# Performance work log

Hardware: AMD Instinct MI355X
Metric: run time of the kernel (lower is better)

The kernel has to match this reference:

```python
import jax, jax.numpy as jnp
import numpy as np

B, N, F_IN = 4, 2048, 256
K, D = 4, 64
NEG_SLOPE = 0.2


def setup_inputs() -> dict:
    key = jax.random.key(0)
    k1, k2, k3, k4, k5 = jax.random.split(key, 5)
    x = jax.random.normal(k1, (B, N, F_IN), dtype=jnp.float32)
    adj = jax.random.randint(k2, (B, N, N), 0, 2, dtype=jnp.int32)
    # xavier_uniform-style params
    def xavier(k, shape):
        fan_in, fan_out = shape[-2], shape[-1]
        lim = np.sqrt(6.0 / (fan_in + fan_out))
        return jax.random.uniform(k, shape, jnp.float32, -lim, lim)
    W = xavier(k3, (K, F_IN, D))
    a_src = xavier(k4, (K, D, 1))
    a_dst = xavier(k5, (K, D, 1))
    return {"x": x, "adj": adj, "W": W, "a_src": a_src, "a_dst": a_dst}


def reference(x, adj, W, a_src, a_dst):
    # Wh: (B, K, N, D)
    Wh = jnp.einsum('bnf,kfd->bknd', x, W)
    e_src = jnp.einsum('bknd,kdo->bkno', Wh, a_src)  # (B,K,N,1)
    e_dst = jnp.einsum('bknd,kdo->bkno', Wh, a_dst)  # (B,K,N,1)
    e = e_src + jnp.swapaxes(e_dst, -2, -1)          # (B,K,N,N)
    e = jnp.where(e > 0, e, NEG_SLOPE * e)           # LeakyReLU(0.2)
    # adjacency mask with forced self-loops (adj + I > 0)
    eye = jnp.eye(e.shape[-1], dtype=bool)
    mask = (adj[:, None, :, :] > 0) | eye            # (B,1|K,N,N)
    e = jnp.where(mask, e, -jnp.inf)
    # numerically-stable softmax matching F_module_softmax
    x_max = jnp.max(e, axis=-1, keepdims=True)
    x_max = jnp.where(jnp.isinf(x_max), 0.0, x_max)
    exp_e = jnp.exp(e - x_max)
    exp_e = jnp.where(jnp.isinf(e), 0.0, exp_e)
    alpha = exp_e / (jnp.sum(exp_e, axis=-1, keepdims=True) + 1e-10)
    # dropout is identity in eval mode
    out = jnp.matmul(alpha, Wh)                      # (B,K,N,D)
    # concat heads: (B,N,K*D)
    Bn, Kn, Nn, Dn = out.shape
    return jnp.transpose(out, (0, 2, 1, 3)).reshape(Bn, Nn, Kn * Dn)
```

## Files before the change

### kernel.cpp

```cpp
#include <hip/hip_runtime.h>

#define NB 4
#define NN 2048
#define NF 256
#define NK 4
#define ND 64
#define NEG 0.2f
#define LOG2E 1.4426950408889634f

typedef _Float16 f16;
typedef _Float16 f16x2 __attribute__((ext_vector_type(2)));
typedef _Float16 f16x4 __attribute__((ext_vector_type(4)));
typedef _Float16 f16x8 __attribute__((ext_vector_type(8)));
typedef float f32x4 __attribute__((ext_vector_type(4)));
typedef float f32x16 __attribute__((ext_vector_type(16)));
typedef unsigned int u32;
typedef unsigned short u16;

__global__ __launch_bounds__(256) void k01(
    const float* __restrict__ x,
    const int*   __restrict__ adj,
    const float* __restrict__ Wm,
    const float* __restrict__ a_src,
    const float* __restrict__ a_dst,
    unsigned int* __restrict__ abit,
    f16* __restrict__ wht,
    float* __restrict__ sbuf,
    f16* __restrict__ ebuf,
    f16* __restrict__ fbuf)
{
    __shared__ f16 wt[64 * 256];

    const int bx  = blockIdx.x;
    const int tid = threadIdx.x;

    if (bx >= 256) {
        const int row = (bx - 256) * 4 + (tid >> 6);
        const int l   = tid & 63;
        const int i   = row & (NN - 1);
        const int* __restrict__ ar = adj + (size_t)row * NN;

        int v[32];
#pragma unroll
        for (int c = 0; c < 32; ++c) v[c] = ar[c * 64 + l];

        unsigned int kx = 0, ky = 0;
#pragma unroll
        for (int c = 0; c < 32; ++c) {
            unsigned long long m = __ballot(v[c] > 0);
            if (l == c) { kx = (unsigned int)m; ky = (unsigned int)(m >> 32); }
        }
        if (l == (i >> 6)) {
            unsigned int sb = 1u << (i & 31);
            if (((i >> 5) & 1) == 0) kx |= sb; else ky |= sb;
        }
        if (l < 32) {
            uint2 kk; kk.x = kx; kk.y = ky;
            *(uint2*)&abit[(size_t)row * 64 + l * 2] = kk;
        }
        return;
    }

    const int gx  = bx & 15;
    const int k   = (bx >> 4) & 3;
    const int b   = bx >> 6;
    const int wv  = tid >> 6;
    const int l   = tid & 63;
    const int q   = l >> 4;
    const int r16 = l & 15;

    for (int fc = 0; fc < 64; ++fc) {
        int f = fc * 4 + wv;
        int d = l;
        wt[d * 256 + (f ^ ((d & 7) << 3))] = (f16)Wm[(k * NF + f) * ND + d];
    }
    __syncthreads();

    const int ncol0 = gx * 128 + wv * 32;
    f32x4 acc[2][4];
#pragma unroll
    for (int nt = 0; nt < 2; ++nt)
#pragma unroll
        for (int dt = 0; dt < 4; ++dt)
            acc[nt][dt] = (f32x4){0.f, 0.f, 0.f, 0.f};

    for (int fs = 0; fs < 16; ++fs) {
        const int f0 = fs * 16 + q * 4;
        f16x4 af[4];
#pragma unroll
        for (int dt = 0; dt < 4; ++dt) {
            int d = dt * 16 + r16;
            af[dt] = *(const f16x4*)&wt[d * 256 + (f0 ^ ((d & 7) << 3))];
        }
#pragma unroll
        for (int nt = 0; nt < 2; ++nt) {
            int n = ncol0 + nt * 16 + r16;
            float4 xv = *(const float4*)&x[((size_t)(b * NN + n)) * NF + f0];
            f16x4 bf = {(f16)xv.x, (f16)xv.y, (f16)xv.z, (f16)xv.w};
#pragma unroll
            for (int dt = 0; dt < 4; ++dt)
                acc[nt][dt] = __builtin_amdgcn_mfma_f32_16x16x16f16(
                    af[dt], bf, acc[nt][dt], 0, 0, 0);
        }
    }

    float asv[4][4], adv[4][4];
#pragma unroll
    for (int dt = 0; dt < 4; ++dt)
#pragma unroll
        for (int rr = 0; rr < 4; ++rr) {
            int d = dt * 16 + q * 4 + rr;
            asv[dt][rr] = a_src[k * ND + d];
            adv[dt][rr] = a_dst[k * ND + d];
        }

    const size_t obase = (size_t)(b * NK + k) * 131072;

#pragma unroll
    for (int nt = 0; nt < 2; ++nt) {
        int n  = ncol0 + nt * 16 + r16;
        const size_t sb_ = obase + (size_t)(n >> 3) * 512 + (n & 7);
        float sp = 0.f, tp = 0.f;
#pragma unroll
        for (int dt = 0; dt < 4; ++dt)
#pragma unroll
            for (int rr = 0; rr < 4; ++rr) {
                float v = acc[nt][dt][rr];
                int d = dt * 16 + q * 4 + rr;
                wht[sb_ + d * 8] = (f16)v;
                sp += v * asv[dt][rr];
                tp += v * adv[dt][rr];
            }
        sp += __shfl_xor(sp, 16);
        sp += __shfl_xor(sp, 32);
        tp += __shfl_xor(tp, 16);
        tp += __shfl_xor(tp, 32);
        if (q == 0) {
            int idx = (b * NK + k) * NN + n;
            sbuf[idx] = sp;
            ebuf[idx] = (f16)__builtin_exp2f(tp * LOG2E);
            fbuf[idx] = (f16)__builtin_exp2f(0.2f * LOG2E * tp);
        }
    }
}

__global__ __launch_bounds__(512, 4) void k2_attn(
    const unsigned int* __restrict__ abit,
    const f16* __restrict__ wht,
    const float* __restrict__ sbuf,
    const f16* __restrict__ ebuf,
    const f16* __restrict__ fbuf,
    float* __restrict__ out)
{
    const int bid = blockIdx.x;
    const int bkv = (bid & 7) | (((bid >> 3) & 1) << 3);
    const int rg  = bid >> 4;
    const int b   = bkv >> 2, k = bkv & 3;
    const int i0  = rg * 64;
    const int tid = threadIdx.x;
    const int w   = tid >> 6;
    const int c   = w >> 1;
    const int rw  = w & 1;
    const int l   = tid & 63;
    const int r32 = l & 31;
    const int hi  = l >> 5;
    const int iglob = i0 + rw * 32 + r32;

    __shared__ __attribute__((aligned(16))) char pool[74752];
    u16* el = (u16*)(pool + 65536);
    u16* fl = (u16*)(pool + 69632);

    const unsigned int* __restrict__ abrow =
        abit + (size_t)(b * NN + iglob) * 64 + c * 16;
    uint2 abx[8];
#pragma unroll
    for (int it = 0; it < 8; ++it) abx[it] = *(const uint2*)(abrow + it * 2);

    {
        const u16* eb = (const u16*)(ebuf + bkv * NN);
        const u16* fb = (const u16*)(fbuf + bkv * NN);
        *(ushort4*)&el[tid * 4] = *(const ushort4*)&eb[tid * 4];
        *(ushort4*)&fl[tid * 4] = *(const ushort4*)&fb[tid * 4];
    }

    const float s   = sbuf[bkv * NN + iglob];
    const f16 Afh = (f16)__builtin_exp2f(0.8f * LOG2E * fminf(s, 0.f));
    const f16 Bfh = (f16)__builtin_exp2f(-0.8f * LOG2E * fmaxf(s, 0.f));
    const f16x2 Af2 = {Afh, Afh};
    const f16x2 Bf2 = {Bfh, Bfh};
    const f16 h1 = (f16)1.0f;
    const f16x8 ones8 = {h1, h1, h1, h1, h1, h1, h1, h1};

    const f16* __restrict__ lanep =
        wht + (size_t)bkv * 131072 + (size_t)(c * 64 + hi) * 512 + r32 * 8;

    f32x16 acc[2], accd;
#pragma unroll
    for (int z = 0; z < 16; ++z) { acc[0][z] = 0.f; acc[1][z] = 0.f; accd[z] = 0.f; }

    __syncthreads();

#pragma unroll
    for (int it = 0; it < 8; ++it) {
        const uint2 ab = abx[it];
#pragma unroll
        for (int jts = 0; jts < 4; ++jts) {
            const u32 word = (jts & 2) ? ab.y : ab.x;
            const u32 bbyte = (word >> (((jts & 1) << 4) + (hi << 3))) & 0xffu;
            const u32 u = (bbyte << 15) | bbyte;
            const int jb = c * 512 + it * 64 + jts * 16 + hi * 8;
            uint4 E4 = *(const uint4*)&el[jb];
            uint4 F4 = *(const uint4*)&fl[jb];
            u32 pa_u[4];
#pragma unroll
            for (int p = 0; p < 4; ++p) {
                f16x2 e2 = __builtin_bit_cast(f16x2, ((const u32*)&E4)[p]);
                f16x2 f2 = __builtin_bit_cast(f16x2, ((const u32*)&F4)[p]);
                f16x2 w2 = __builtin_elementwise_max(Af2 * e2, Bf2 * f2);
                u32 x  = (u >> (2 * p)) & 0x00010001u;
                u32 mm = (x << 16) - x;
                pa_u[p] = __builtin_bit_cast(u32, w2) & mm;
            }
            uint4 pav = {pa_u[0], pa_u[1], pa_u[2], pa_u[3]};
            f16x8 pa = __builtin_bit_cast(f16x8, pav);

            const f16* fp = lanep + (size_t)(it * 8 + jts * 2) * 512;
            f16x8 v80 = *(const f16x8*)(fp);
            f16x8 v81 = *(const f16x8*)(fp + 256);
            acc[0] = __builtin_amdgcn_mfma_f32_32x32x16_f16(pa, v80, acc[0], 0, 0, 0);
            acc[1] = __builtin_amdgcn_mfma_f32_32x32x16_f16(pa, v81, acc[1], 0, 0, 0);
            accd   = __builtin_amdgcn_mfma_f32_32x32x16_f16(pa, ones8, accd, 0, 0, 0);
        }
    }

    __syncthreads();
    float* stash = (float*)pool;
    if (c != 0) {
        float* sb = stash + ((c - 1) * 2 + rw) * 3072 + l * 48;
#pragma unroll
        for (int dh = 0; dh < 2; ++dh)
#pragma unroll
            for (int sub = 0; sub < 4; ++sub) {
                f32x4 v = {acc[dh][sub * 4], acc[dh][sub * 4 + 1],
                           acc[dh][sub * 4 + 2], acc[dh][sub * 4 + 3]};
                *(f32x4*)&sb[dh * 16 + ((sub ^ (l & 3)) << 2)] = v;
            }
#pragma unroll
        for (int sub = 0; sub < 4; ++sub) {
            f32x4 v = {accd[sub * 4], accd[sub * 4 + 1],
                       accd[sub * 4 + 2], accd[sub * 4 + 3]};
            *(f32x4*)&sb[32 + ((sub ^ (l & 3)) << 2)] = v;
        }
    }
    __syncthreads();

    if (c == 0) {
#pragma unroll
        for (int cc = 0; cc < 3; ++cc) {
            const float* sr = stash + (cc * 2 + rw) * 3072 + l * 48;
#pragma unroll
            for (int dh = 0; dh < 2; ++dh)
#pragma unroll
                for (int sub = 0; sub < 4; ++sub) {
                    f32x4 v = *(const f32x4*)&sr[dh * 16 + ((sub ^ (l & 3)) << 2)];
#pragma unroll
                    for (int m = 0; m < 4; ++m) acc[dh][sub * 4 + m] += v[m];
                }
#pragma unroll
            for (int sub = 0; sub < 4; ++sub) {
                f32x4 v = *(const f32x4*)&sr[32 + ((sub ^ (l & 3)) << 2)];
#pragma unroll
                for (int m = 0; m < 4; ++m) accd[sub * 4 + m] += v[m];
            }
        }
        float* op = out + ((size_t)(b * NN) + i0 + rw * 32) * (NK * ND) + k * ND;
#pragma unroll
        for (int g4 = 0; g4 < 4; ++g4)
#pragma unroll
            for (int m = 0; m < 4; ++m) {
                const int rr   = g4 * 4 + m;
                const int irow = g4 * 8 + hi * 4 + m;
                const float inv = 1.f / (accd[rr] + 1e-10f);
                op[(size_t)irow * (NK * ND) + r32]      = acc[0][rr] * inv;
                op[(size_t)irow * (NK * ND) + 32 + r32] = acc[1][rr] * inv;
            }
    }
}

extern "C" void kernel_launch(void* const* d_in, const int* in_sizes, int n_in,
                              void* d_out, int out_size, void* d_ws, size_t ws_size,
                              hipStream_t stream) {
    const float* x     = (const float*)d_in[0];
    const int*   adj   = (const int*)d_in[1];
    const float* Wm    = (const float*)d_in[2];
    const float* a_src = (const float*)d_in[3];
    const float* a_dst = (const float*)d_in[4];
    float* out = (float*)d_out;

    char* ws = (char*)d_ws;
    f16*   wht  = (f16*)ws;
    float* sbuf = (float*)(ws + (4u << 20));
    f16*   ebuf = (f16*)(ws + (4u << 20) + (128u << 10));
    f16*   fbuf = (f16*)(ws + (4u << 20) + (192u << 10));
    unsigned int* abit = (unsigned int*)(ws + (4u << 20) + (256u << 10));

    k01<<<dim3(256 + NB * NN / 4), 256, 0, stream>>>(
        x, adj, Wm, a_src, a_dst, abit, wht, sbuf, ebuf, fbuf);
    k2_attn<<<dim3(512), 512, 0, stream>>>(
        abit, wht, sbuf, ebuf, fbuf, out);
}
```

Measured before the change: 41.64 us.

## Restructure attention kernel to 4 waves covering both row halves with LDS atomic reduction

The attention kernel now uses 256 threads, with each wave owning one quarter of the j-range and computing both 32-row halves. Each V fragment loaded from global memory therefore feeds two pairs of MFMAs instead of one pair. The ones-vector MFMA that computed the softmax denominator is replaced by packed fdot2 sums in VALU, and the cross-wave reduction now uses LDS float atomicAdd into a shared accumulator instead of the register stash plus c==0 reduction. This increases V reuse and cuts the MFMA count, but adds VALU work, 64 LDS atomics per lane, and higher register pressure from four accumulators.

New measurement: 83.62 us. 101% more time.

```diff
diff --git a/kernel.cpp b/kernel.cpp
--- a/kernel.cpp
+++ b/kernel.cpp
@@ -144,7 +144,7 @@
     }
 }
 
-__global__ __launch_bounds__(512, 4) void k2_attn(
+__global__ __launch_bounds__(256, 4) void k2_attn(
     const unsigned int* __restrict__ abit,
     const f16* __restrict__ wht,
     const float* __restrict__ sbuf,
@@ -159,131 +159,126 @@
     const int i0  = rg * 64;
     const int tid = threadIdx.x;
     const int w   = tid >> 6;
-    const int c   = w >> 1;
-    const int rw  = w & 1;
     const int l   = tid & 63;
     const int r32 = l & 31;
     const int hi  = l >> 5;
-    const int iglob = i0 + rw * 32 + r32;
-
-    __shared__ __attribute__((aligned(16))) char pool[74752];
-    u16* el = (u16*)(pool + 65536);
-    u16* fl = (u16*)(pool + 69632);
-
-    const unsigned int* __restrict__ abrow =
-        abit + (size_t)(b * NN + iglob) * 64 + c * 16;
-    uint2 abx[8];
-#pragma unroll
-    for (int it = 0; it < 8; ++it) abx[it] = *(const uint2*)(abrow + it * 2);
-
+    const int row_a = i0 + r32;
+    const int row_b = i0 + 32 + r32;
+
+    __shared__ __attribute__((aligned(16))) char pool[24832];
+    float* accbuf = (float*)pool;
+    float* dden   = (float*)(pool + 16384);
+    u16*   el     = (u16*)(pool + 16640);
+    u16*   fl     = (u16*)(pool + 20736);
+
+#pragma unroll
+    for (int z = 0; z < 17; ++z) {
+        int idx = z * 256 + tid;
+        if (idx < 4160) accbuf[idx] = 0.f;
+    }
     {
         const u16* eb = (const u16*)(ebuf + bkv * NN);
         const u16* fb = (const u16*)(fbuf + bkv * NN);
-        *(ushort4*)&el[tid * 4] = *(const ushort4*)&eb[tid * 4];
-        *(ushort4*)&fl[tid * 4] = *(const ushort4*)&fb[tid * 4];
-    }
-
-    const float s   = sbuf[bkv * NN + iglob];
-    const f16 Afh = (f16)__builtin_exp2f(0.8f * LOG2E * fminf(s, 0.f));
-    const f16 Bfh = (f16)__builtin_exp2f(-0.8f * LOG2E * fmaxf(s, 0.f));
-    const f16x2 Af2 = {Afh, Afh};
-    const f16x2 Bf2 = {Bfh, Bfh};
-    const f16 h1 = (f16)1.0f;
-    const f16x8 ones8 = {h1, h1, h1, h1, h1, h1, h1, h1};
+        *(uint4*)&el[tid * 8] = *(const uint4*)&eb[tid * 8];
+        *(uint4*)&fl[tid * 8] = *(const uint4*)&fb[tid * 8];
+    }
+
+    const float s_a = sbuf[bkv * NN + row_a];
+    const float s_b = sbuf[bkv * NN + row_b];
+    const f16 Afa = (f16)__builtin_exp2f(0.8f * LOG2E * fminf(s_a, 0.f));
+    const f16 Bfa = (f16)__builtin_exp2f(-0.8f * LOG2E * fmaxf(s_a, 0.f));
+    const f16 Afb = (f16)__builtin_exp2f(0.8f * LOG2E * fminf(s_b, 0.f));
+    const f16 Bfb = (f16)__builtin_exp2f(-0.8f * LOG2E * fmaxf(s_b, 0.f));
+    const f16x2 Af2a = {Afa, Afa}, Bf2a = {Bfa, Bfa};
+    const f16x2 Af2b = {Afb, Afb}, Bf2b = {Bfb, Bfb};
+    const f16x2 one2 = {(f16)1.0f, (f16)1.0f};
+
+    const unsigned int* __restrict__ abrow_a =
+        abit + (size_t)(b * NN + row_a) * 64 + w * 16;
+    const unsigned int* __restrict__ abrow_b = abrow_a + 32 * 64;
 
     const f16* __restrict__ lanep =
-        wht + (size_t)bkv * 131072 + (size_t)(c * 64 + hi) * 512 + r32 * 8;
-
-    f32x16 acc[2], accd;
-#pragma unroll
-    for (int z = 0; z < 16; ++z) { acc[0][z] = 0.f; acc[1][z] = 0.f; accd[z] = 0.f; }
+        wht + (size_t)bkv * 131072 + (size_t)(w * 64 + hi) * 512 + r32 * 8;
+
+    float den_a = 0.f, den_b = 0.f;
+    f32x16 acc[4];
+#pragma unroll
+    for (int t = 0; t < 4; ++t)
+#pragma unroll
+        for (int z = 0; z < 16; ++z) acc[t][z] = 0.f;
 
     __syncthreads();
 
+#define PABUILD(PA, DEN, AF2, BF2, WORD)                                       \
+    do {                                                                       \
+        const u32 bbyte = ((WORD) >> (((jts & 1) << 4) + (hi << 3))) & 0xffu;  \
+        const u32 u = (bbyte << 15) | bbyte;                                   \
+        u32 pa_u[4];                                                           \
+        _Pragma("unroll") for (int p = 0; p < 4; ++p) {                        \
+            f16x2 e2 = __builtin_bit_cast(f16x2, ((const u32*)&E4)[p]);        \
+            f16x2 f2 = __builtin_bit_cast(f16x2, ((const u32*)&F4)[p]);        \
+            f16x2 w2 = __builtin_elementwise_max((AF2) * e2, (BF2) * f2);      \
+            u32 xx = (u >> (2 * p)) & 0x00010001u;                             \
+            u32 mm = (xx << 16) - xx;                                          \
+            pa_u[p] = __builtin_bit_cast(u32, w2) & mm;                        \
+            DEN = __builtin_amdgcn_fdot2(                                      \
+                __builtin_bit_cast(f16x2, pa_u[p]), one2, DEN, false);         \
+        }                                                                      \
+        uint4 pav = {pa_u[0], pa_u[1], pa_u[2], pa_u[3]};                      \
+        PA = __builtin_bit_cast(f16x8, pav);                                   \
+    } while (0)
+
 #pragma unroll
     for (int it = 0; it < 8; ++it) {
-        const uint2 ab = abx[it];
+        const uint2 ab_a = *(const uint2*)(abrow_a + it * 2);
+        const uint2 ab_b = *(const uint2*)(abrow_b + it * 2);
 #pragma unroll
         for (int jts = 0; jts < 4; ++jts) {
-            const u32 word = (jts & 2) ? ab.y : ab.x;
-            const u32 bbyte = (word >> (((jts & 1) << 4) + (hi << 3))) & 0xffu;
-            const u32 u = (bbyte << 15) | bbyte;
-            const int jb = c * 512 + it * 64 + jts * 16 + hi * 8;
+            const int jb = w * 512 + it * 64 + jts * 16 + hi * 8;
             uint4 E4 = *(const uint4*)&el[jb];
             uint4 F4 = *(const uint4*)&fl[jb];
-            u32 pa_u[4];
-#pragma unroll
-            for (int p = 0; p < 4; ++p) {
-                f16x2 e2 = __builtin_bit_cast(f16x2, ((const u32*)&E4)[p]);
-                f16x2 f2 = __builtin_bit_cast(f16x2, ((const u32*)&F4)[p]);
-                f16x2 w2 = __builtin_elementwise_max(Af2 * e2, Bf2 * f2);
-                u32 x  = (u >> (2 * p)) & 0x00010001u;
-                u32 mm = (x << 16) - x;
-                pa_u[p] = __builtin_bit_cast(u32, w2) & mm;
-            }
-            uint4 pav = {pa_u[0], pa_u[1], pa_u[2], pa_u[3]};
-            f16x8 pa = __builtin_bit_cast(f16x8, pav);
+            const u32 word_a = (jts & 2) ? ab_a.y : ab_a.x;
+            const u32 word_b = (jts & 2) ? ab_b.y : ab_b.x;
+            f16x8 pa_a, pa_b;
+            PABUILD(pa_a, den_a, Af2a, Bf2a, word_a);
+            PABUILD(pa_b, den_b, Af2b, Bf2b, word_b);
 
             const f16* fp = lanep + (size_t)(it * 8 + jts * 2) * 512;
             f16x8 v80 = *(const f16x8*)(fp);
             f16x8 v81 = *(const f16x8*)(fp + 256);
-            acc[0] = __builtin_amdgcn_mfma_f32_32x32x16_f16(pa, v80, acc[0], 0, 0, 0);
-            acc[1] = __builtin_amdgcn_mfma_f32_32x32x16_f16(pa, v81, acc[1], 0, 0, 0);
-            accd   = __builtin_amdgcn_mfma_f32_32x32x16_f16(pa, ones8, accd, 0, 0, 0);
-        }
-    }
-
+            acc[0] = __builtin_amdgcn_mfma_f32_32x32x16_f16(pa_a, v80, acc[0], 0, 0, 0);
+            acc[1] = __builtin_amdgcn_mfma_f32_32x32x16_f16(pa_a, v81, acc[1], 0, 0, 0);
+            acc[2] = __builtin_amdgcn_mfma_f32_32x32x16_f16(pa_b, v80, acc[2], 0, 0, 0);
+            acc[3] = __builtin_amdgcn_mfma_f32_32x32x16_f16(pa_b, v81, acc[3], 0, 0, 0);
+        }
+    }
+#undef PABUILD
+
+    den_a += __shfl_xor(den_a, 32);
+    den_b += __shfl_xor(den_b, 32);
+    if (hi == 0) {
+        atomicAdd(&dden[r32], den_a);
+        atomicAdd(&dden[32 + r32], den_b);
+    }
+
+#pragma unroll
+    for (int t = 0; t < 4; ++t) {
+        const int rbase = (t >> 1) * 32 + hi * 4;
+        const int d = (t & 1) * 32 + r32;
+#pragma unroll
+        for (int rr = 0; rr < 16; ++rr) {
+            const int row = rbase + (rr & 3) + 8 * (rr >> 2);
+            atomicAdd(&accbuf[row * 64 + d], acc[t][rr]);
+        }
+    }
     __syncthreads();
-    float* stash = (float*)pool;
-    if (c != 0) {
-        float* sb = stash + ((c - 1) * 2 + rw) * 3072 + l * 48;
-#pragma unroll
-        for (int dh = 0; dh < 2; ++dh)
-#pragma unroll
-            for (int sub = 0; sub < 4; ++sub) {
-                f32x4 v = {acc[dh][sub * 4], acc[dh][sub * 4 + 1],
-                           acc[dh][sub * 4 + 2], acc[dh][sub * 4 + 3]};
-                *(f32x4*)&sb[dh * 16 + ((sub ^ (l & 3)) << 2)] = v;
-            }
-#pragma unroll
-        for (int sub = 0; sub < 4; ++sub) {
-            f32x4 v = {accd[sub * 4], accd[sub * 4 + 1],
-                       accd[sub * 4 + 2], accd[sub * 4 + 3]};
-            *(f32x4*)&sb[32 + ((sub ^ (l & 3)) << 2)] = v;
-        }
-    }
-    __syncthreads();
-
-    if (c == 0) {
-#pragma unroll
-        for (int cc = 0; cc < 3; ++cc) {
-            const float* sr = stash + (cc * 2 + rw) * 3072 + l * 48;
-#pragma unroll
-            for (int dh = 0; dh < 2; ++dh)
-#pragma unroll
-                for (int sub = 0; sub < 4; ++sub) {
-                    f32x4 v = *(const f32x4*)&sr[dh * 16 + ((sub ^ (l & 3)) << 2)];
-#pragma unroll
-                    for (int m = 0; m < 4; ++m) acc[dh][sub * 4 + m] += v[m];
-                }
-#pragma unroll
-            for (int sub = 0; sub < 4; ++sub) {
-                f32x4 v = *(const f32x4*)&sr[32 + ((sub ^ (l & 3)) << 2)];
-#pragma unroll
-                for (int m = 0; m < 4; ++m) accd[sub * 4 + m] += v[m];
-            }
-        }
-        float* op = out + ((size_t)(b * NN) + i0 + rw * 32) * (NK * ND) + k * ND;
-#pragma unroll
-        for (int g4 = 0; g4 < 4; ++g4)
-#pragma unroll
-            for (int m = 0; m < 4; ++m) {
-                const int rr   = g4 * 4 + m;
-                const int irow = g4 * 8 + hi * 4 + m;
-                const float inv = 1.f / (accd[rr] + 1e-10f);
-                op[(size_t)irow * (NK * ND) + r32]      = acc[0][rr] * inv;
-                op[(size_t)irow * (NK * ND) + 32 + r32] = acc[1][rr] * inv;
-            }
+
+    float* op = out + ((size_t)(b * NN) + i0) * (NK * ND) + k * ND;
+#pragma unroll
+    for (int r = 0; r < 16; ++r) {
+        const int row = w * 16 + r;
+        const float inv = 1.f / (dden[row] + 1e-10f);
+        op[(size_t)row * (NK * ND) + l] = accbuf[row * 64 + l] * inv;
     }
 }
 
@@ -306,6 +301,6 @@
 
     k01<<<dim3(256 + NB * NN / 4), 256, 0, stream>>>(
         x, adj, Wm, a_src, a_dst, abit, wht, sbuf, ebuf, fbuf);
-    k2_attn<<<dim3(512), 512, 0, stream>>>(
+    k2_attn<<<dim3(512), 256, 0, stream>>>(
         abit, wht, sbuf, ebuf, fbuf, out);
 }
```

## Split attention across 8 column waves with LDS atomic reduction and fdot2 denominator

Applied to the files above, without the earlier changes.

Each block of k2_attn now handles 32 rows instead of 64, and all 8 waves split the 2048 columns into 256-column chunks. The grid doubles to 1024 blocks and LDS use shrinks from about 73KB to 16KB, which should allow more blocks per CU. The row-sum denominator is now computed with fdot2 on the masked weights instead of a third MFMA against a ones vector. Partial results are combined with LDS float atomicAdds rather than the staged stash-and-sum, which adds atomic contention and makes the reduction order nondeterministic.

Result: slower. 119.8 us (+187.8%).

```diff
diff --git a/kernel.cpp b/kernel.cpp
--- a/kernel.cpp
+++ b/kernel.cpp
@@ -144,7 +144,7 @@
     }
 }
 
-__global__ __launch_bounds__(512, 4) void k2_attn(
+__global__ __launch_bounds__(512) void k2_attn(
     const unsigned int* __restrict__ abit,
     const f16* __restrict__ wht,
     const float* __restrict__ sbuf,
@@ -153,62 +153,67 @@
     float* __restrict__ out)
 {
     const int bid = blockIdx.x;
-    const int bkv = (bid & 7) | (((bid >> 3) & 1) << 3);
+    const int bkv = bid & 15;
     const int rg  = bid >> 4;
     const int b   = bkv >> 2, k = bkv & 3;
-    const int i0  = rg * 64;
+    const int i0  = rg * 32;
     const int tid = threadIdx.x;
     const int w   = tid >> 6;
-    const int c   = w >> 1;
-    const int rw  = w & 1;
     const int l   = tid & 63;
     const int r32 = l & 31;
     const int hi  = l >> 5;
-    const int iglob = i0 + rw * 32 + r32;
-
-    __shared__ __attribute__((aligned(16))) char pool[74752];
-    u16* el = (u16*)(pool + 65536);
-    u16* fl = (u16*)(pool + 69632);
-
-    const unsigned int* __restrict__ abrow =
-        abit + (size_t)(b * NN + iglob) * 64 + c * 16;
-    uint2 abx[8];
-#pragma unroll
-    for (int it = 0; it < 8; ++it) abx[it] = *(const uint2*)(abrow + it * 2);
-
+    const int iglob = i0 + r32;
+
+    __shared__ __attribute__((aligned(16))) char pool[16512];
+    float* accbuf = (float*)pool;
+    float* dden   = (float*)(pool + 8192);
+    u16*   el     = (u16*)(pool + 8320);
+    u16*   fl     = (u16*)(pool + 12416);
+
+#pragma unroll
+    for (int z = 0; z < 5; ++z) {
+        int idx = z * 512 + tid;
+        if (idx < 2080) accbuf[idx] = 0.f;
+    }
     {
         const u16* eb = (const u16*)(ebuf + bkv * NN);
         const u16* fb = (const u16*)(fbuf + bkv * NN);
-        *(ushort4*)&el[tid * 4] = *(const ushort4*)&eb[tid * 4];
-        *(ushort4*)&fl[tid * 4] = *(const ushort4*)&fb[tid * 4];
-    }
-
-    const float s   = sbuf[bkv * NN + iglob];
+        *(uint2*)&el[tid * 4] = *(const uint2*)&eb[tid * 4];
+        *(uint2*)&fl[tid * 4] = *(const uint2*)&fb[tid * 4];
+    }
+
+    const unsigned int* __restrict__ abrow =
+        abit + (size_t)(b * NN + iglob) * 64 + w * 8;
+    uint2 abx[4];
+#pragma unroll
+    for (int it = 0; it < 4; ++it) abx[it] = *(const uint2*)(abrow + it * 2);
+
+    const float s  = sbuf[bkv * NN + iglob];
     const f16 Afh = (f16)__builtin_exp2f(0.8f * LOG2E * fminf(s, 0.f));
     const f16 Bfh = (f16)__builtin_exp2f(-0.8f * LOG2E * fmaxf(s, 0.f));
     const f16x2 Af2 = {Afh, Afh};
     const f16x2 Bf2 = {Bfh, Bfh};
-    const f16 h1 = (f16)1.0f;
-    const f16x8 ones8 = {h1, h1, h1, h1, h1, h1, h1, h1};
+    const f16x2 one2 = {(f16)1.0f, (f16)1.0f};
 
     const f16* __restrict__ lanep =
-        wht + (size_t)bkv * 131072 + (size_t)(c * 64 + hi) * 512 + r32 * 8;
-
-    f32x16 acc[2], accd;
-#pragma unroll
-    for (int z = 0; z < 16; ++z) { acc[0][z] = 0.f; acc[1][z] = 0.f; accd[z] = 0.f; }
+        wht + (size_t)bkv * 131072 + (size_t)(w * 32 + hi) * 512 + r32 * 8;
+
+    float den = 0.f;
+    f32x16 acc[2];
+#pragma unroll
+    for (int z = 0; z < 16; ++z) { acc[0][z] = 0.f; acc[1][z] = 0.f; }
 
     __syncthreads();
 
 #pragma unroll
-    for (int it = 0; it < 8; ++it) {
+    for (int it = 0; it < 4; ++it) {
         const uint2 ab = abx[it];
 #pragma unroll
         for (int jts = 0; jts < 4; ++jts) {
             const u32 word = (jts & 2) ? ab.y : ab.x;
             const u32 bbyte = (word >> (((jts & 1) << 4) + (hi << 3))) & 0xffu;
             const u32 u = (bbyte << 15) | bbyte;
-            const int jb = c * 512 + it * 64 + jts * 16 + hi * 8;
+            const int jb = w * 256 + it * 64 + jts * 16 + hi * 8;
             uint4 E4 = *(const uint4*)&el[jb];
             uint4 F4 = *(const uint4*)&fl[jb];
             u32 pa_u[4];
@@ -217,9 +222,11 @@
                 f16x2 e2 = __builtin_bit_cast(f16x2, ((const u32*)&E4)[p]);
                 f16x2 f2 = __builtin_bit_cast(f16x2, ((const u32*)&F4)[p]);
                 f16x2 w2 = __builtin_elementwise_max(Af2 * e2, Bf2 * f2);
-                u32 x  = (u >> (2 * p)) & 0x00010001u;
-                u32 mm = (x << 16) - x;
+                u32 xx = (u >> (2 * p)) & 0x00010001u;
+                u32 mm = (xx << 16) - xx;
                 pa_u[p] = __builtin_bit_cast(u32, w2) & mm;
+                den = __builtin_amdgcn_fdot2(
+                    __builtin_bit_cast(f16x2, pa_u[p]), one2, den, false);
             }
             uint4 pav = {pa_u[0], pa_u[1], pa_u[2], pa_u[3]};
             f16x8 pa = __builtin_bit_cast(f16x8, pav);
@@ -229,61 +236,29 @@
             f16x8 v81 = *(const f16x8*)(fp + 256);
             acc[0] = __builtin_amdgcn_mfma_f32_32x32x16_f16(pa, v80, acc[0], 0, 0, 0);
             acc[1] = __builtin_amdgcn_mfma_f32_32x32x16_f16(pa, v81, acc[1], 0, 0, 0);
-            accd   = __builtin_amdgcn_mfma_f32_32x32x16_f16(pa, ones8, accd, 0, 0, 0);
-        }
-    }
-
+        }
+    }
+
+    den += __shfl_xor(den, 32);
+    if (hi == 0) atomicAdd(&dden[r32], den);
+
+#pragma unroll
+    for (int dh = 0; dh < 2; ++dh) {
+        const int d = dh * 32 + r32;
+#pragma unroll
+        for (int rr = 0; rr < 16; ++rr) {
+            const int row = (rr & 3) + 8 * (rr >> 2) + 4 * hi;
+            atomicAdd(&accbuf[row * 64 + d], acc[dh][rr]);
+        }
+    }
     __syncthreads();
-    float* stash = (float*)pool;
-    if (c != 0) {
-        float* sb = stash + ((c - 1) * 2 + rw) * 3072 + l * 48;
-#pragma unroll
-        for (int dh = 0; dh < 2; ++dh)
-#pragma unroll
-            for (int sub = 0; sub < 4; ++sub) {
-                f32x4 v = {acc[dh][sub * 4], acc[dh][sub * 4 + 1],
-                           acc[dh][sub * 4 + 2], acc[dh][sub * 4 + 3]};
-                *(f32x4*)&sb[dh * 16 + ((sub ^ (l & 3)) << 2)] = v;
-            }
-#pragma unroll
-        for (int sub = 0; sub < 4; ++sub) {
-            f32x4 v = {accd[sub * 4], accd[sub * 4 + 1],
-                       accd[sub * 4 + 2], accd[sub * 4 + 3]};
-            *(f32x4*)&sb[32 + ((sub ^ (l & 3)) << 2)] = v;
-        }
-    }
-    __syncthreads();
-
-    if (c == 0) {
-#pragma unroll
-        for (int cc = 0; cc < 3; ++cc) {
-            const float* sr = stash + (cc * 2 + rw) * 3072 + l * 48;
-#pragma unroll
-            for (int dh = 0; dh < 2; ++dh)
-#pragma unroll
-                for (int sub = 0; sub < 4; ++sub) {
-                    f32x4 v = *(const f32x4*)&sr[dh * 16 + ((sub ^ (l & 3)) << 2)];
-#pragma unroll
-                    for (int m = 0; m < 4; ++m) acc[dh][sub * 4 + m] += v[m];
-                }
-#pragma unroll
-            for (int sub = 0; sub < 4; ++sub) {
-                f32x4 v = *(const f32x4*)&sr[32 + ((sub ^ (l & 3)) << 2)];
-#pragma unroll
-                for (int m = 0; m < 4; ++m) accd[sub * 4 + m] += v[m];
-            }
-        }
-        float* op = out + ((size_t)(b * NN) + i0 + rw * 32) * (NK * ND) + k * ND;
-#pragma unroll
-        for (int g4 = 0; g4 < 4; ++g4)
-#pragma unroll
-            for (int m = 0; m < 4; ++m) {
-                const int rr   = g4 * 4 + m;
-                const int irow = g4 * 8 + hi * 4 + m;
-                const float inv = 1.f / (accd[rr] + 1e-10f);
-                op[(size_t)irow * (NK * ND) + r32]      = acc[0][rr] * inv;
-                op[(size_t)irow * (NK * ND) + 32 + r32] = acc[1][rr] * inv;
-            }
+
+    float* op = out + ((size_t)(b * NN) + i0) * (NK * ND) + k * ND;
+#pragma unroll
+    for (int r = 0; r < 4; ++r) {
+        const int row = w * 4 + r;
+        const float inv = 1.f / (dden[row] + 1e-10f);
+        op[(size_t)row * (NK * ND) + l] = accbuf[row * 64 + l] * inv;
     }
 }
 
@@ -306,6 +281,6 @@
 
     k01<<<dim3(256 + NB * NN / 4), 256, 0, stream>>>(
         x, adj, Wm, a_src, a_dst, abit, wht, sbuf, ebuf, fbuf);
-    k2_attn<<<dim3(512), 512, 0, stream>>>(
+    k2_attn<<<dim3(1024), 512, 0, stream>>>(
         abit, wht, sbuf, ebuf, fbuf, out);
 }
```
